# Performance work log

Hardware: AMD Instinct MI355X
Metric: run time of the kernel (lower is better)

The kernel has to match this reference:

```python
import jax, jax.numpy as jnp
import numpy as np

B = 36          # fixed batch_size in source
T = 60          # time_window
DECAY = 0.3     # LIAF default decay
THRESH = 0.5    # LIAF default firing threshold


def conv3x3(x, W, b):
    # x: [B,C,H,W], W: [O,C,3,3], padding=1, stride=1
    y = jax.lax.conv_general_dilated(x, W, (1, 1), [(1, 1), (1, 1)],
                                     dimension_numbers=('NCHW', 'OIHW', 'NCHW'))
    return y + b[None, :, None, None]


def avgpool2(x):
    # 2x2 average pool, stride 2
    b, c, h, w = x.shape
    return x.reshape(b, c, h // 2, 2, w // 2, 2).mean(axis=(3, 5))


def liaf(u, spike, mem):
    # leaky-integrate with spike-gated reset, analog (ReLU) fire
    mem = mem * DECAY * (1.0 - spike) + u
    new_spike = (mem > THRESH).astype(mem.dtype)
    out = jax.nn.relu(mem)
    return new_spike, mem, out


def setup_inputs() -> dict:
    key = jax.random.key(0)
    ks = jax.random.split(key, 8)
    # DVS event frames in [0,3) so the >1 binarization keeps ~2/3 of pixels
    data = (jax.random.uniform(ks[0], (B, 2, 32, 32, T)) * 3.0).astype(jnp.float32)

    def w(k, shape, fan_in):
        return (jax.random.normal(k, shape) * (1.0 / np.sqrt(fan_in))).astype(jnp.float32)

    return dict(
        data=data,
        win=T,
        W0=w(ks[1], (64, 2, 3, 3), 2 * 9), b0=jnp.zeros((64,), jnp.float32),
        W1=w(ks[2], (128, 64, 3, 3), 64 * 9), b1=jnp.zeros((128,), jnp.float32),
        W2=w(ks[3], (128, 128, 3, 3), 128 * 9), b2=jnp.zeros((128,), jnp.float32),
        Wf1=w(ks[4], (256, 8192), 8192), bf1=jnp.zeros((256,), jnp.float32),
        Wf2=w(ks[5], (11, 256), 256), bf2=jnp.zeros((11,), jnp.float32),
    )


def reference(data, W0, b0, W1, b1, W2, b2, Wf1, bf1, Wf2, bf2, win):
    dtype = data.dtype
    z = lambda s: jnp.zeros(s, dtype)
    # (spike, mem) pairs for every LIAF cell + output-spike accumulator
    state0 = (
        (z((B, 64, 32, 32)), z((B, 64, 32, 32))),   # c0
        (z((B, 128, 32, 32)), z((B, 128, 32, 32))), # c1
        (z((B, 128, 16, 16)), z((B, 128, 16, 16))), # p1
        (z((B, 128, 16, 16)), z((B, 128, 16, 16))), # c2
        (z((B, 128, 8, 8)), z((B, 128, 8, 8))),     # p2
        (z((B, 256)), z((B, 256))),                 # h1
        (z((B, 11)), z((B, 11))),                   # h2
        z((B, 11)),                                 # sum of analog outputs
    )
    xs = jnp.moveaxis(data, -1, 0)[:win]

    def step(st, xt):
        c0, c1, p1, c2, p2, h1, h2, acc = st
        x = (xt > 1.0).astype(dtype)  # binarize accumulated frame
        s, m, out = liaf(conv3x3(x, W0, b0), *c0); c0 = (s, m)
        s, m, out = liaf(conv3x3(out, W1, b1), *c1); c1 = (s, m)
        s, m, out = liaf(avgpool2(out), *p1); p1 = (s, m)
        s, m, out = liaf(conv3x3(out, W2, b2), *c2); c2 = (s, m)
        s, m, out = liaf(avgpool2(out), *p2); p2 = (s, m)
        out = out.reshape(B, -1)  # [B, 8*8*128]
        s, m, out = liaf(out @ Wf1.T + bf1, *h1); h1 = (s, m)
        s, m, out = liaf(out @ Wf2.T + bf2, *h2); h2 = (s, m)
        return (c0, c1, p1, c2, p2, h1, h2, acc + out), None

    st_f, _ = jax.lax.scan(step, state0, xs)
    return st_f[-1] / T
```

## Files before the change

kernel.cpp:

```cpp
#include <hip/hip_runtime.h>

#define NB 36
#define NT 60

typedef __attribute__((ext_vector_type(8))) short short8;
typedef __attribute__((ext_vector_type(4))) float f32x4;

struct Params {
  const float *data;
  const float *W0, *b0, *W1, *b1, *W2, *b2, *Wf1, *bf1, *Wf2, *bf2;
  float *xb, *w0t;
  unsigned short *w1h, *w1l, *w2h, *w2l;
  unsigned int *xhl, *p1hl;
  float *outp2, *u1s;
  float *dm0, *dm1, *dmp1, *dm2, *dmp2, *dmh1, *dmh2;
  float *acc;
  float *zbase; int zn4;
};

__device__ __forceinline__ unsigned short bf16_rne(float v){
  unsigned int bits = __float_as_uint(v);
  unsigned int r = bits + 0x7FFFu + ((bits >> 16) & 1u);
  return (unsigned short)(r >> 16);
}
__device__ __forceinline__ unsigned int bf16pack(float v){
  unsigned short h = bf16_rne(v);
  float hf = __uint_as_float((unsigned int)h << 16);
  unsigned short l = bf16_rne(v - hf);
  return (unsigned int)h | ((unsigned int)l << 16);
}
__device__ __forceinline__ void unpack8(const unsigned int* q, short8& h8, short8& l8){
  unsigned int u[8];
  *(uint4*)&u[0] = *(const uint4*)q;
  *(uint4*)&u[4] = *(const uint4*)(q+4);
  #pragma unroll
  for(int i=0;i<8;i++){
    h8[i] = (short)(u[i] & 0xffffu);
    l8[i] = (short)(u[i] >> 16);
  }
}

__global__ void __launch_bounds__(256) k_prep(Params p){
  int gt  = blockIdx.x*256 + threadIdx.x;
  int STR = gridDim.x*256;
  if(gt < NB*11) p.acc[gt] = 0.f;
  for(int i=gt; i<p.zn4; i+=STR) ((float4*)p.zbase)[i] = make_float4(0.f,0.f,0.f,0.f);
  const int PLANE = 34*34;
  for(int i=gt; i<NT*NB*2*PLANE; i+=STR){
    int t   = i / (NB*2*PLANE);
    int rem = i % (NB*2*PLANE);
    int bc  = rem / PLANE;
    int pix = rem % PLANE;
    int ph = pix/34, pw = pix%34;
    float v = 0.f;
    if(ph>=1 && ph<=32 && pw>=1 && pw<=32){
      float d = p.data[((size_t)bc*1024 + (ph-1)*32 + (pw-1))*NT + t];
      v = (d > 1.0f) ? 1.0f : 0.0f;
    }
    p.xb[i] = v;
  }
  for(int i=gt; i<2*9*64; i+=STR){
    int co=i%64, rr=i/64; p.w0t[i] = p.W0[(co*2 + rr/9)*9 + rr%9];
  }
  for(int i=gt; i<128*576; i+=STR){
    int co = i/576, k = i%576;
    int cin = k/9, dd = k%9;
    unsigned int pk = bf16pack(p.W1[(co*64+cin)*9 + dd]);
    p.w1h[i]=(unsigned short)(pk&0xffffu); p.w1l[i]=(unsigned short)(pk>>16);
  }
  for(int i=gt; i<128*1152; i+=STR){
    int co = i/1152, k = i%1152;
    int cin = k/9, dd = k%9;
    unsigned int pk = bf16pack(p.W2[(co*128+cin)*9 + dd]);
    p.w2h[i]=(unsigned short)(pk&0xffffu); p.w2l[i]=(unsigned short)(pk>>16);
  }
}

template<int Cin,int Cout,int HW,int CO,int PX,int TY,int CS>
__global__ void __launch_bounds__(HW*TY)
k_conv0(const float* __restrict__ x, const float* __restrict__ wt,
        const float* __restrict__ bias, float* __restrict__ dm,
        unsigned int* __restrict__ outhl)
{
  const int NCOG = Cout/CO;
  const int TH   = PX*TY;
  const int NHG  = HW/TH;
  const int NH4  = CO/4;
  const int NTHL = HW*TY;
  const int PIN  = HW+2;
  const int XR   = PX+2;
  int tile = blockIdx.x;
  int tid  = threadIdx.x;
  int cog = tile % NCOG;
  int hg  = (tile/NCOG) % NHG;
  int b   = tile/(NCOG*NHG);
  int w0  = tid % HW;
  int ty  = tid / HW;
  int h0  = hg*TH + ty*PX;

  __shared__ __align__(16) float wl[CS*9*CO];

  float accs[PX][CO];
  #pragma unroll
  for(int p=0;p<PX;p++)
    #pragma unroll
    for(int c=0;c<CO;c++) accs[p][c]=0.f;

  for(int cs=0; cs<Cin; cs+=CS){
    __syncthreads();
    for(int j=tid; j<CS*9*CO; j+=NTHL){
      int c  = j % CO;
      int rr = j / CO;
      wl[j] = wt[(cs*9 + rr)*Cout + cog*CO + c];
    }
    __syncthreads();

    for(int lc=0; lc<CS; lc++){
      const float* xc = x + ((size_t)b*Cin + cs + lc)*PIN*PIN + (size_t)h0*PIN + w0;
      float xv[XR][3];
      #pragma unroll
      for(int r=0;r<XR;r++)
        #pragma unroll
        for(int c=0;c<3;c++) xv[r][c] = xc[(size_t)r*PIN + c];
      const float4* w4 = (const float4*)(wl + lc*9*CO);
      #pragma unroll
      for(int dh=0;dh<3;dh++){
        #pragma unroll
        for(int g=0;g<NH4;g++){
          float4 wa = w4[(dh*3+0)*NH4+g];
          float4 wb = w4[(dh*3+1)*NH4+g];
          float4 wc = w4[(dh*3+2)*NH4+g];
          const float* A  = (const float*)&wa;
          const float* Bp = (const float*)&wb;
          const float* Cp = (const float*)&wc;
          #pragma unroll
          for(int cc=0;cc<4;cc++){
            #pragma unroll
            for(int px=0;px<PX;px++)
              accs[px][g*4+cc] += A[cc]*xv[px+dh][0] + Bp[cc]*xv[px+dh][1] + Cp[cc]*xv[px+dh][2];
          }
        }
      }
    }
  }

  int co0 = cog*CO;
  #pragma unroll
  for(int co=0; co<CO; co++){
    float bsv = bias[co0+co];
    const int OS = HW + 2;
    size_t plane = (size_t)(b*Cout + co0+co)*OS*OS;
    #pragma unroll
    for(int px=0; px<PX; px++){
      size_t idx = plane + (size_t)(h0+px+1)*OS + w0 + 1;
      float mem = dm[idx] + accs[px][co] + bsv;
      float ov = mem > 0.f ? mem : 0.f;
      dm[idx]  = (mem > 0.5f) ? 0.f : 0.3f*mem;
      outhl[idx] = bf16pack(ov);
    }
  }
}

__global__ void __launch_bounds__(256, 4)
k_conv1(const unsigned int* __restrict__ xhl,
        const unsigned short* __restrict__ w1h, const unsigned short* __restrict__ w1l,
        const float* __restrict__ bias, float* __restrict__ dm,
        float* __restrict__ dmp, unsigned int* __restrict__ p1hl)
{
  __shared__ __align__(16) unsigned int ldsu[5376];
  unsigned short* Ah = (unsigned short*)ldsu;
  unsigned short* Al = (unsigned short*)(ldsu + 1280);
  unsigned int*   Xp = ldsu + 2560;

  int bid = blockIdx.x;
  int cog = bid & 1;
  int pxg = (bid>>1) & 15;
  int b   = bid >> 5;
  int tid = threadIdx.x;
  int wv  = tid >> 6, lane = tid & 63;
  int wm = wv & 1, wn = wv >> 1;
  int n = lane & 15, quad = lane >> 4;
  int r0 = pxg*2;

  f32x4 acc[2][2];
  #pragma unroll
  for(int mo=0;mo<2;mo++)
    #pragma unroll
    for(int no=0;no<2;no++) acc[mo][no] = (f32x4){0.f,0.f,0.f,0.f};

  int aco = tid >> 2;
  int aq  = tid & 3;
  const unsigned short* whp = w1h + (size_t)(cog*64 + aco)*576 + aq*8;
  const unsigned short* wlp = w1l + (size_t)(cog*64 + aco)*576 + aq*8;
  int sk  = tid >> 3;
  int pxq = tid & 7;
  int srow = pxq >> 2;
  int scol = (pxq & 3) * 8;
  int rA   = pxq * 8;
  int skx  = sk ^ (((pxq >> 1) & 3) << 3);

  uint4 wha = *(const uint4*)(whp);
  uint4 wla = *(const uint4*)(wlp);
  unsigned int tmp[8];
  {
    int cin = sk / 9;
    int dd  = sk - cin*9;
    int dh = dd/3, dw = dd - dh*3;
    const unsigned int* sx = xhl + ((size_t)(b*64 + cin)*34 + (r0 + srow + dh))*34 + scol + dw;
    #pragma unroll
    for(int i=0;i<8;i++) tmp[i] = sx[i];
  }

  for(int ch=0; ch<18; ch++){
    __syncthreads();
    *(uint4*)&Ah[aco*40 + aq*8] = wha;
    *(uint4*)&Al[aco*40 + aq*8] = wla;
    #pragma unroll
    for(int i=0;i<8;i++) Xp[(rA+i)*44 + skx] = tmp[i];
    __syncthreads();

    if(ch+1 < 18){
      int k0n = (ch+1)*32;
      wha = *(const uint4*)(whp + k0n);
      wla = *(const uint4*)(wlp + k0n);
      int kg = k0n + sk;
      int cin = kg / 9;
      int dd  = kg - cin*9;
      int dh = dd/3, dw = dd - dh*3;
      const unsigned int* sx = xhl + ((size_t)(b*64 + cin)*34 + (r0 + srow + dh))*34 + scol + dw;
      #pragma unroll
      for(int i=0;i<8;i++) tmp[i] = sx[i];
    }

    short8 ahf[2], alf[2];
    #pragma unroll
    for(int mo=0;mo<2;mo++){
      int row = wm*32 + mo*16 + n;
      ahf[mo] = *(const short8*)&Ah[row*40 + quad*8];
      alf[mo] = *(const short8*)&Al[row*40 + quad*8];
    }
    #pragma unroll
    for(int no=0;no<2;no++){
      int prow = no*32 + wn*16 + n;
      int cb = ((quad ^ (no*2 + wn)) & 3) * 8;
      short8 xhf, xlf;
      unpack8(&Xp[prow*44 + cb], xhf, xlf);
      #pragma unroll
      for(int mo=0;mo<2;mo++){
        acc[mo][no] = __builtin_amdgcn_mfma_f32_16x16x32_bf16(ahf[mo], xhf, acc[mo][no],0,0,0);
        acc[mo][no] = __builtin_amdgcn_mfma_f32_16x16x32_bf16(ahf[mo], xlf, acc[mo][no],0,0,0);
        acc[mo][no] = __builtin_amdgcn_mfma_f32_16x16x32_bf16(alf[mo], xhf, acc[mo][no],0,0,0);
      }
    }
  }

  #pragma unroll
  for(int mo=0;mo<2;mo++){
    #pragma unroll
    for(int reg=0;reg<4;reg++){
      int co = cog*64 + wm*32 + mo*16 + quad*4 + reg;
      float bsv = bias[co];
      float o[2];
      #pragma unroll
      for(int no=0;no<2;no++){
        int r = r0 + no;
        int c = wn*16 + n;
        size_t idx = (((size_t)b*128 + co)*32 + r)*32 + c;
        float mem = dm[idx] + acc[mo][no][reg] + bsv;
        o[no] = mem > 0.f ? mem : 0.f;
        dm[idx] = (mem > 0.5f) ? 0.f : 0.3f*mem;
      }
      float s = o[0] + o[1];
      s += __shfl_xor(s, 1, 64);
      if((n&1)==0){
        int pr = pxg;
        int pc = wn*8 + (n>>1);
        size_t pidx = (((size_t)b*128 + co)*18 + pr+1)*18 + pc+1;
        float pm = dmp[pidx] + s*0.25f;
        float pv = pm > 0.f ? pm : 0.f;
        dmp[pidx] = (pm > 0.5f) ? 0.f : 0.3f*pm;
        p1hl[pidx] = bf16pack(pv);
      }
    }
  }
}

__global__ void __launch_bounds__(256, 4)
k_x2(const unsigned int* __restrict__ p1hl,
     const unsigned short* __restrict__ w2h, const unsigned short* __restrict__ w2l,
     const float* __restrict__ bias2, float* __restrict__ dm2,
     float* __restrict__ dmp2, float* __restrict__ outp,
     const float* __restrict__ xnext, const float* __restrict__ w0t,
     const float* __restrict__ bias0, float* __restrict__ dm0,
     unsigned int* __restrict__ xhl, int do_c0,
     const float* __restrict__ u1s, const float* __restrict__ bf1,
     const float* __restrict__ Wf2, const float* __restrict__ bf2,
     float* __restrict__ dmh1, float* __restrict__ dmh2,
     float* __restrict__ accv, int do_fc2)
{
  __shared__ __align__(16) unsigned int ldsu[3968];
  const int tid = threadIdx.x;
  int bid = blockIdx.x;

  if(bid >= 864){
    if(!do_fc2) return;
    float* xs = (float*)ldsu;
    int b = bid - 864;
    int o = tid;
    float u = bf1[o];
    const float* pu = u1s + (size_t)b*256 + o;
    #pragma unroll
    for(int s=0;s<32;s++) u += pu[(size_t)s*NB*256];
    int idx = b*256 + o;
    float mem = dmh1[idx] + u;
    float xo = mem > 0.f ? mem : 0.f;
    dmh1[idx] = (mem > 0.5f) ? 0.f : 0.3f*mem;
    xs[o] = xo;
    __syncthreads();
    int w_id = o >> 6, ln = o & 63;
    for(int oo=w_id; oo<11; oo+=4){
      const float* wr = Wf2 + oo*256;
      float s = xs[ln]*wr[ln] + xs[ln+64]*wr[ln+64]
              + xs[ln+128]*wr[ln+128] + xs[ln+192]*wr[ln+192];
      #pragma unroll
      for(int off=32; off>0; off>>=1) s += __shfl_down(s, off, 64);
      if(ln==0){
        int i2 = b*11 + oo;
        float m2 = dmh2[i2] + s + bf2[oo];
        float ov = m2 > 0.f ? m2 : 0.f;
        dmh2[i2] = (m2 > 0.5f) ? 0.f : 0.3f*m2;
        accv[i2] += ov * (1.0f/60.0f);
      }
    }
    return;
  }

  if(bid >= 576){
    if(!do_c0) return;
    float* wl = (float*)ldsu;
    int tile = bid - 576;
    int cog = tile & 7;
    int b   = tile >> 3;
    int w0  = tid & 31;
    int ty  = tid >> 5;
    int h0  = ty*4;

    float accs[4][8];
    #pragma unroll
    for(int p=0;p<4;p++)
      #pragma unroll
      for(int c=0;c<8;c++) accs[p][c]=0.f;

    if(tid < 144){
      int c  = tid % 8;
      int rr = tid / 8;
      wl[tid] = w0t[rr*64 + cog*8 + c];
    }
    __syncthreads();

    #pragma unroll
    for(int lc=0; lc<2; lc++){
      const float* xc = xnext + ((size_t)b*2 + lc)*34*34 + (size_t)h0*34 + w0;
      float xv[6][3];
      #pragma unroll
      for(int r=0;r<6;r++)
        #pragma unroll
        for(int c=0;c<3;c++) xv[r][c] = xc[(size_t)r*34 + c];
      const float4* w4 = (const float4*)(wl + lc*72);
      #pragma unroll
      for(int dh=0;dh<3;dh++){
        #pragma unroll
        for(int g=0;g<2;g++){
          float4 wa = w4[(dh*3+0)*2+g];
          float4 wb = w4[(dh*3+1)*2+g];
          float4 wc = w4[(dh*3+2)*2+g];
          const float* A  = (const float*)&wa;
          const float* Bp = (const float*)&wb;
          const float* Cp = (const float*)&wc;
          #pragma unroll
          for(int cc=0;cc<4;cc++){
            #pragma unroll
            for(int px=0;px<4;px++)
              accs[px][g*4+cc] += A[cc]*xv[px+dh][0] + Bp[cc]*xv[px+dh][1] + Cp[cc]*xv[px+dh][2];
          }
        }
      }
    }

    int co0 = cog*8;
    #pragma unroll
    for(int co=0; co<8; co++){
      float bsv = bias0[co0+co];
      size_t plane = (size_t)(b*64 + co0+co)*34*34;
      #pragma unroll
      for(int px=0; px<4; px++){
        size_t idx = plane + (size_t)(h0+px+1)*34 + w0 + 1;
        float mem = dm0[idx] + accs[px][co] + bsv;
        float ov = mem > 0.f ? mem : 0.f;
        dm0[idx]  = (mem > 0.5f) ? 0.f : 0.3f*mem;
        xhl[idx] = bf16pack(ov);
      }
    }
    return;
  }

  unsigned short* Ah = (unsigned short*)ldsu;
  unsigned short* Al = (unsigned short*)(ldsu + 1280);
  unsigned int*   Xp = ldsu + 2560;

  int cog = bid & 1;
  int pxg = (bid>>1) & 7;
  int b   = bid >> 4;
  int wv  = tid >> 6, lane = tid & 63;
  int wm = wv & 1, wn = wv >> 1;
  int n = lane & 15, quad = lane >> 4;
  int r0 = pxg*2;

  f32x4 acc2[2];
  #pragma unroll
  for(int mo=0;mo<2;mo++) acc2[mo] = (f32x4){0.f,0.f,0.f,0.f};

  int aco = tid >> 2;
  int aq  = tid & 3;
  const unsigned short* whp = w2h + (size_t)(cog*64 + aco)*1152 + aq*8;
  const unsigned short* wlp = w2l + (size_t)(cog*64 + aco)*1152 + aq*8;
  int sk  = tid >> 3;
  int pxq = tid & 7;
  int srow = pxq >> 2;
  int scol = (pxq & 3) * 4;
  int rA   = pxq * 4;
  int skx  = sk ^ ((pxq >> 2) << 3);

  uint4 wha = *(const uint4*)(whp);
  uint4 wla = *(const uint4*)(wlp);
  unsigned int tmp[4];
  {
    int cin = sk / 9;
    int dd  = sk - cin*9;
    int dh = dd/3, dw = dd - dh*3;
    const unsigned int* sx = p1hl + ((size_t)(b*128 + cin)*18 + (r0 + srow + dh))*18 + scol + dw;
    #pragma unroll
    for(int i=0;i<4;i++) tmp[i] = sx[i];
  }

  for(int ch=0; ch<36; ch++){
    __syncthreads();
    *(uint4*)&Ah[aco*40 + aq*8] = wha;
    *(uint4*)&Al[aco*40 + aq*8] = wla;
    #pragma unroll
    for(int i=0;i<4;i++) Xp[(rA+i)*44 + skx] = tmp[i];
    __syncthreads();

    if(ch+1 < 36){
      int k0n = (ch+1)*32;
      wha = *(const uint4*)(whp + k0n);
      wla = *(const uint4*)(wlp + k0n);
      int kg = k0n + sk;
      int cin = kg / 9;
      int dd  = kg - cin*9;
      int dh = dd/3, dw = dd - dh*3;
      const unsigned int* sx = p1hl + ((size_t)(b*128 + cin)*18 + (r0 + srow + dh))*18 + scol + dw;
      #pragma unroll
      for(int i=0;i<4;i++) tmp[i] = sx[i];
    }

    short8 ahf[2], alf[2];
    #pragma unroll
    for(int mo=0;mo<2;mo++){
      int row = wm*32 + mo*16 + n;
      ahf[mo] = *(const short8*)&Ah[row*40 + quad*8];
      alf[mo] = *(const short8*)&Al[row*40 + quad*8];
    }
    {
      int prow = (n>>3)*16 + wn*8 + (n&7);
      int cb = ((quad ^ (n>>3)) & 3) * 8;
      short8 xhf, xlf;
      unpack8(&Xp[prow*44 + cb], xhf, xlf);
      #pragma unroll
      for(int mo=0;mo<2;mo++){
        acc2[mo] = __builtin_amdgcn_mfma_f32_16x16x32_bf16(ahf[mo], xhf, acc2[mo],0,0,0);
        acc2[mo] = __builtin_amdgcn_mfma_f32_16x16x32_bf16(ahf[mo], xlf, acc2[mo],0,0,0);
        acc2[mo] = __builtin_amdgcn_mfma_f32_16x16x32_bf16(alf[mo], xhf, acc2[mo],0,0,0);
      }
    }
  }

  #pragma unroll
  for(int mo=0;mo<2;mo++){
    #pragma unroll
    for(int reg=0;reg<4;reg++){
      int co = cog*64 + wm*32 + mo*16 + quad*4 + reg;
      float bsv = bias2[co];
      int r = r0 + (n>>3);
      int c = wn*8 + (n&7);
      size_t idx = (((size_t)b*128 + co)*16 + r)*16 + c;
      float mem = dm2[idx] + acc2[mo][reg] + bsv;
      float o = mem > 0.f ? mem : 0.f;
      dm2[idx] = (mem > 0.5f) ? 0.f : 0.3f*mem;
      float s = o;
      s += __shfl_xor(s, 8, 64);
      s += __shfl_xor(s, 1, 64);
      if((n & 9) == 0){
        int pr = pxg;
        int pc = wn*4 + ((n&7)>>1);
        size_t pidx = (((size_t)b*128 + co)*8 + pr)*8 + pc;
        float pm = dmp2[pidx] + s*0.25f;
        outp[pidx] = pm > 0.f ? pm : 0.f;
        dmp2[pidx]  = (pm > 0.5f) ? 0.f : 0.3f*pm;
      }
    }
  }
}

__global__ void __launch_bounds__(256)
k_fc1(const float* __restrict__ X, const float* __restrict__ Wf,
      float* __restrict__ u1s){
  __shared__ __align__(16) float lds[4896];
  float* Wl = lds;
  float* Xl = lds + 32*68;
  const int tid = threadIdx.x;
  int ot = blockIdx.x & 7, ks = blockIdx.x >> 3;
  int o0 = ot*32, k0 = ks*256;
  int w_id = tid >> 6, lane = tid & 63;
  int o_l = lane & 7, bg = lane >> 3;
  float acc[4][5];
  #pragma unroll
  for(int i=0;i<4;i++)
    #pragma unroll
    for(int j=0;j<5;j++) acc[i][j]=0.f;

  for(int c=0; c<4; c++){
    int kb = k0 + c*64;
    __syncthreads();
    for(int idx=tid; idx<512; idx+=256){
      int r = idx >> 4, j = idx & 15;
      *(float4*)&Wl[r*68 + j*4] = *(const float4*)&Wf[(size_t)(o0+r)*8192 + kb + j*4];
    }
    for(int idx=tid; idx<640; idx+=256){
      int r = idx >> 4, j = idx & 15;
      float4 v = make_float4(0.f,0.f,0.f,0.f);
      if(r < NB) v = *(const float4*)&X[(size_t)r*8192 + kb + j*4];
      *(float4*)&Xl[r*68 + j*4] = v;
    }
    __syncthreads();
    #pragma unroll
    for(int c4=0; c4<4; c4++){
      int g = w_id*4 + c4;
      float4 wv[4], xv[5];
      #pragma unroll
      for(int oi=0;oi<4;oi++) wv[oi] = *(const float4*)&Wl[(o_l+8*oi)*68 + g*4];
      #pragma unroll
      for(int bi=0;bi<5;bi++) xv[bi] = *(const float4*)&Xl[(bg*5+bi)*68 + g*4];
      #pragma unroll
      for(int oi=0;oi<4;oi++)
        #pragma unroll
        for(int bi=0;bi<5;bi++)
          acc[oi][bi] += wv[oi].x*xv[bi].x + wv[oi].y*xv[bi].y
                       + wv[oi].z*xv[bi].z + wv[oi].w*xv[bi].w;
    }
  }
  __syncthreads();
  if(w_id > 0){
    float* r = lds + ((w_id-1)*64 + lane)*20;
    #pragma unroll
    for(int oi=0;oi<4;oi++)
      #pragma unroll
      for(int bi=0;bi<5;bi++) r[oi*5+bi] = acc[oi][bi];
  }
  __syncthreads();
  if(w_id == 0){
    #pragma unroll
    for(int wv=0;wv<3;wv++){
      float* r = lds + (wv*64 + lane)*20;
      #pragma unroll
      for(int oi=0;oi<4;oi++)
        #pragma unroll
        for(int bi=0;bi<5;bi++) acc[oi][bi] += r[oi*5+bi];
    }
    #pragma unroll
    for(int bi=0;bi<5;bi++){
      int b = bg*5 + bi;
      if(b < NB){
        #pragma unroll
        for(int oi=0;oi<4;oi++)
          u1s[((size_t)ks*NB + b)*256 + o0 + o_l + 8*oi] = acc[oi][bi];
      }
    }
  }
}

__global__ void __launch_bounds__(256)
k_fc2(const float* __restrict__ u1s, const float* __restrict__ bf1,
      const float* __restrict__ Wf2, const float* __restrict__ bf2,
      float* __restrict__ dmh1, float* __restrict__ dmh2, float* __restrict__ acc){
  __shared__ float xs[256];
  int b = blockIdx.x;
  int o = threadIdx.x;
  float u = bf1[o];
  const float* p = u1s + (size_t)b*256 + o;
  #pragma unroll
  for(int s=0;s<32;s++) u += p[(size_t)s*NB*256];
  int idx = b*256 + o;
  float mem = dmh1[idx] + u;
  float xo = mem > 0.f ? mem : 0.f;
  dmh1[idx] = (mem > 0.5f) ? 0.f : 0.3f*mem;
  xs[o] = xo;
  __syncthreads();
  int w_id = o >> 6, lane = o & 63;
  for(int oo=w_id; oo<11; oo+=4){
    const float* wr = Wf2 + oo*256;
    float s = xs[lane]*wr[lane] + xs[lane+64]*wr[lane+64]
            + xs[lane+128]*wr[lane+128] + xs[lane+192]*wr[lane+192];
    #pragma unroll
    for(int off=32; off>0; off>>=1) s += __shfl_down(s, off, 64);
    if(lane==0){
      int i2 = b*11 + oo;
      float m2 = dmh2[i2] + s + bf2[oo];
      float ov = m2 > 0.f ? m2 : 0.f;
      dmh2[i2] = (m2 > 0.5f) ? 0.f : 0.3f*m2;
      acc[i2] += ov * (1.0f/60.0f);
    }
  }
}

extern "C" void kernel_launch(void* const* d_in, const int* in_sizes, int n_in,
                              void* d_out, int out_size, void* d_ws, size_t ws_size,
                              hipStream_t stream) {
  Params p;
  p.data = (const float*)d_in[0];
  p.W0  = (const float*)d_in[2];  p.b0  = (const float*)d_in[3];
  p.W1  = (const float*)d_in[4];  p.b1  = (const float*)d_in[5];
  p.W2  = (const float*)d_in[6];  p.b2  = (const float*)d_in[7];
  p.Wf1 = (const float*)d_in[8];  p.bf1 = (const float*)d_in[9];
  p.Wf2 = (const float*)d_in[10]; p.bf2 = (const float*)d_in[11];
  p.acc = (float*)d_out;

  float* ws = (float*)d_ws;
  const size_t S_XB    = (size_t)NT*NB*2*34*34;
  const size_t S_W0T   = 2*9*64;
  const size_t S_W1S   = 128*576/2;
  const size_t S_W2S   = 128*1152/2;
  const size_t S_XHL   = (size_t)NB*64*34*34;
  const size_t S_P1HL  = (size_t)NB*128*18*18;
  const size_t S_OP2   = (size_t)NB*128*8*8;
  const size_t S_U1S   = (size_t)32*NB*256;
  const size_t S_DM0   = (size_t)NB*64*34*34;
  const size_t S_DM1   = (size_t)NB*128*32*32;
  const size_t S_DMP1  = (size_t)NB*128*18*18;
  const size_t S_DM2   = (size_t)NB*128*16*16;
  const size_t S_DMP2  = S_OP2;
  const size_t S_OH1   = (size_t)NB*256;

  p.xb    = ws;  ws += S_XB;
  p.w0t   = ws;  ws += S_W0T;
  p.w1h   = (unsigned short*)ws;  ws += S_W1S;
  p.w1l   = (unsigned short*)ws;  ws += S_W1S;
  p.w2h   = (unsigned short*)ws;  ws += S_W2S;
  p.w2l   = (unsigned short*)ws;  ws += S_W2S;
  p.zbase = ws;
  p.xhl   = (unsigned int*)ws;    ws += S_XHL;
  p.p1hl  = (unsigned int*)ws;    ws += S_P1HL;
  p.outp2 = ws;  ws += S_OP2;
  p.u1s   = ws;  ws += S_U1S;
  p.dm0   = ws;  ws += S_DM0;
  p.dm1   = ws;  ws += S_DM1;
  p.dmp1  = ws;  ws += S_DMP1;
  p.dm2   = ws;  ws += S_DM2;
  p.dmp2  = ws;  ws += S_DMP2;
  p.dmh1  = ws;  ws += S_OH1;
  p.dmh2  = ws;  ws += (size_t)NB*11;
  p.zn4   = (int)((ws - p.zbase) / 4);

  k_prep<<<dim3(1024), dim3(256), 0, stream>>>(p);
  k_conv0<2,64,32,8,4,8,2><<<dim3(288), dim3(256), 0, stream>>>(
      p.xb, p.w0t, p.b0, p.dm0, p.xhl);
  for(int t=0; t<NT; t++){
    k_conv1<<<dim3(1152), dim3(256), 0, stream>>>(
        p.xhl, p.w1h, p.w1l, p.b1, p.dm1, p.dmp1, p.p1hl);
    const float* xnext = p.xb + (size_t)(t+1)*NB*2*34*34;
    k_x2<<<dim3(900), dim3(256), 0, stream>>>(
        p.p1hl, p.w2h, p.w2l, p.b2, p.dm2, p.dmp2, p.outp2,
        xnext, p.w0t, p.b0, p.dm0, p.xhl, t < NT-1 ? 1 : 0,
        p.u1s, p.bf1, p.Wf2, p.bf2, p.dmh1, p.dmh2, p.acc, t > 0 ? 1 : 0);
    k_fc1<<<dim3(256), dim3(256), 0, stream>>>(p.outp2, p.Wf1, p.u1s);
  }
  k_fc2<<<dim3(36), dim3(256), 0, stream>>>(p.u1s, p.bf1, p.Wf2, p.bf2,
                                            p.dmh1, p.dmh2, p.acc);
}
```

Baseline: 5.259 ms.

## Fuse FC1 split-K blocks into conv1 launch to cut per-step kernel launches

FC1 for the previous timestep now runs as 256 extra blocks appended to the conv1 launch, since conv1 does not depend on FC1. This removes one kernel launch and its serialization point per timestep and lets FC1 overlap with conv1 work. A final standalone FC1 launch after the loop handles the last step. The FC1 blocks share conv1's LDS size and launch bounds, so they may run with a less tuned configuration than the standalone kernel.

```diff
diff --git a/kernel.cpp b/kernel.cpp
--- a/kernel.cpp
+++ b/kernel.cpp
@@ -162,21 +162,101 @@
 }
 
 __global__ void __launch_bounds__(256, 4)
-k_conv1(const unsigned int* __restrict__ xhl,
-        const unsigned short* __restrict__ w1h, const unsigned short* __restrict__ w1l,
-        const float* __restrict__ bias, float* __restrict__ dm,
-        float* __restrict__ dmp, unsigned int* __restrict__ p1hl)
+k_x1(const unsigned int* __restrict__ xhl,
+     const unsigned short* __restrict__ w1h, const unsigned short* __restrict__ w1l,
+     const float* __restrict__ bias, float* __restrict__ dm,
+     float* __restrict__ dmp, unsigned int* __restrict__ p1hl,
+     const float* __restrict__ X, const float* __restrict__ Wf,
+     float* __restrict__ u1s, int do_fc1)
 {
   __shared__ __align__(16) unsigned int ldsu[5376];
+  const int tid = threadIdx.x;
+  int bid = blockIdx.x;
+
+  if(bid >= 1152){
+    if(!do_fc1) return;
+    float* lds = (float*)ldsu;
+    float* Wl = lds;
+    float* Xl = lds + 32*68;
+    int bq = bid - 1152;
+    int ot = bq & 7, ks = bq >> 3;
+    int o0 = ot*32, k0 = ks*256;
+    int w_id = tid >> 6, lane = tid & 63;
+    int o_l = lane & 7, bg = lane >> 3;
+    float acc[4][5];
+    #pragma unroll
+    for(int i=0;i<4;i++)
+      #pragma unroll
+      for(int j=0;j<5;j++) acc[i][j]=0.f;
+
+    for(int c=0; c<4; c++){
+      int kb = k0 + c*64;
+      __syncthreads();
+      for(int idx=tid; idx<512; idx+=256){
+        int r = idx >> 4, j = idx & 15;
+        *(float4*)&Wl[r*68 + j*4] = *(const float4*)&Wf[(size_t)(o0+r)*8192 + kb + j*4];
+      }
+      for(int idx=tid; idx<640; idx+=256){
+        int r = idx >> 4, j = idx & 15;
+        float4 v = make_float4(0.f,0.f,0.f,0.f);
+        if(r < NB) v = *(const float4*)&X[(size_t)r*8192 + kb + j*4];
+        *(float4*)&Xl[r*68 + j*4] = v;
+      }
+      __syncthreads();
+      #pragma unroll
+      for(int c4=0; c4<4; c4++){
+        int g = w_id*4 + c4;
+        float4 wv[4], xv[5];
+        #pragma unroll
+        for(int oi=0;oi<4;oi++) wv[oi] = *(const float4*)&Wl[(o_l+8*oi)*68 + g*4];
+        #pragma unroll
+        for(int bi=0;bi<5;bi++) xv[bi] = *(const float4*)&Xl[(bg*5+bi)*68 + g*4];
+        #pragma unroll
+        for(int oi=0;oi<4;oi++)
+          #pragma unroll
+          for(int bi=0;bi<5;bi++)
+            acc[oi][bi] += wv[oi].x*xv[bi].x + wv[oi].y*xv[bi].y
+                         + wv[oi].z*xv[bi].z + wv[oi].w*xv[bi].w;
+      }
+    }
+    __syncthreads();
+    if(w_id > 0){
+      float* r = lds + ((w_id-1)*64 + lane)*20;
+      #pragma unroll
+      for(int oi=0;oi<4;oi++)
+        #pragma unroll
+        for(int bi=0;bi<5;bi++) r[oi*5+bi] = acc[oi][bi];
+    }
+    __syncthreads();
+    if(w_id == 0){
+      #pragma unroll
+      for(int wv=0;wv<3;wv++){
+        float* r = lds + (wv*64 + lane)*20;
+        #pragma unroll
+        for(int oi=0;oi<4;oi++)
+          #pragma unroll
+          for(int bi=0;bi<5;bi++) acc[oi][bi] += r[oi*5+bi];
+      }
+      #pragma unroll
+      for(int bi=0;bi<5;bi++){
+        int b = bg*5 + bi;
+        if(b < NB){
+          #pragma unroll
+          for(int oi=0;oi<4;oi++)
+            u1s[((size_t)ks*NB + b)*256 + o0 + o_l + 8*oi] = acc[oi][bi];
+        }
+      }
+    }
+    return;
+  }
+
   unsigned short* Ah = (unsigned short*)ldsu;
   unsigned short* Al = (unsigned short*)(ldsu + 1280);
   unsigned int*   Xp = ldsu + 2560;
 
-  int bid = blockIdx.x;
   int cog = bid & 1;
   int pxg = (bid>>1) & 15;
   int b   = bid >> 5;
-  int tid = threadIdx.x;
   int wv  = tid >> 6, lane = tid & 63;
   int wm = wv & 1, wn = wv >> 1;
   int n = lane & 15, quad = lane >> 4;
@@ -675,15 +755,16 @@
   k_conv0<2,64,32,8,4,8,2><<<dim3(288), dim3(256), 0, stream>>>(
       p.xb, p.w0t, p.b0, p.dm0, p.xhl);
   for(int t=0; t<NT; t++){
-    k_conv1<<<dim3(1152), dim3(256), 0, stream>>>(
-        p.xhl, p.w1h, p.w1l, p.b1, p.dm1, p.dmp1, p.p1hl);
+    k_x1<<<dim3(1408), dim3(256), 0, stream>>>(
+        p.xhl, p.w1h, p.w1l, p.b1, p.dm1, p.dmp1, p.p1hl,
+        p.outp2, p.Wf1, p.u1s, t > 0 ? 1 : 0);
     const float* xnext = p.xb + (size_t)(t+1)*NB*2*34*34;
     k_x2<<<dim3(900), dim3(256), 0, stream>>>(
         p.p1hl, p.w2h, p.w2l, p.b2, p.dm2, p.dmp2, p.outp2,
         xnext, p.w0t, p.b0, p.dm0, p.xhl, t < NT-1 ? 1 : 0,
         p.u1s, p.bf1, p.Wf2, p.bf2, p.dmh1, p.dmh2, p.acc, t > 0 ? 1 : 0);
-    k_fc1<<<dim3(256), dim3(256), 0, stream>>>(p.outp2, p.Wf1, p.u1s);
-  }
+  }
+  k_fc1<<<dim3(256), dim3(256), 0, stream>>>(p.outp2, p.Wf1, p.u1s);
   k_fc2<<<dim3(36), dim3(256), 0, stream>>>(p.u1s, p.bf1, p.Wf2, p.bf2,
                                             p.dmh1, p.dmh2, p.acc);
 }
```

Result: slower. 6.900 ms (+31.2%).
